# Performance work log

Measured on AMD Instinct MI355X. Metric: run time of the kernel, lower is better.

Reference implementation:

```python
import jax, jax.numpy as jnp
import numpy as np

DIM = 256
NUM_HEADS = 4
HEAD_DIM = DIM // NUM_HEADS
EPS = 1e-5


def setup_inputs() -> dict:
    key = jax.random.key(0)
    ks = jax.random.split(key, 8)
    B, N, C = 8, 2048, DIM
    s = 0.02
    return {
        "x": jax.random.normal(ks[0], (B, N, C), jnp.float32),
        "qkv_w": jax.random.normal(ks[1], (C, 3 * C), jnp.float32) * s,
        "qkv_b": jnp.zeros((3 * C,), jnp.float32),
        "proj_w": jax.random.normal(ks[2], (C, C), jnp.float32) * s,
        "proj_b": jnp.zeros((C,), jnp.float32),
        "ln1_g": jnp.ones((C,), jnp.float32),
        "ln1_b": jnp.zeros((C,), jnp.float32),
        "ln2_g": jnp.ones((C,), jnp.float32),
        "ln2_b": jnp.zeros((C,), jnp.float32),
        "mlp_w1": jax.random.normal(ks[3], (C, 2 * C), jnp.float32) * s,
        "mlp_b1": jnp.zeros((2 * C,), jnp.float32),
        "mlp_w2": jax.random.normal(ks[4], (2 * C, C), jnp.float32) * s,
        "mlp_b2": jnp.zeros((C,), jnp.float32),
    }


def _layernorm(x, g, b):
    mu = jnp.mean(x, axis=-1, keepdims=True)
    var = jnp.mean(jnp.square(x - mu), axis=-1, keepdims=True)
    return (x - mu) * jax.lax.rsqrt(var + EPS) * g + b


def reference(x, qkv_w, qkv_b, proj_w, proj_b, ln1_g, ln1_b, ln2_g, ln2_b,
              mlp_w1, mlp_b1, mlp_w2, mlp_b2):
    B, N, C = x.shape
    H, D = NUM_HEADS, HEAD_DIM
    shortcut = x
    h = _layernorm(x, ln1_g, ln1_b)
    qkv = (h @ qkv_w + qkv_b).reshape(B, N, 3, H, D)
    q = qkv[:, :, 0].transpose(0, 2, 1, 3)  # [B,H,N,D]
    k = qkv[:, :, 1].transpose(0, 2, 1, 3)
    v = qkv[:, :, 2].transpose(0, 2, 1, 3)
    attn = jnp.einsum('bhnd,bhmd->bhnm', q, k) * (D ** -0.5)
    attn = jax.nn.softmax(attn, axis=-1)  # dropout = identity (eval mode)
    o = jnp.einsum('bhnm,bhmd->bhnd', attn, v)
    o = o.transpose(0, 2, 1, 3).reshape(B, N, C)
    x = o @ proj_w + proj_b + shortcut
    h2 = _layernorm(x, ln2_g, ln2_b)
    mlp = jax.nn.gelu(h2 @ mlp_w1 + mlp_b1, approximate=False) @ mlp_w2 + mlp_b2
    return x + mlp
```

## Files before the change

### kernel.cpp

```cpp
#include <hip/hip_runtime.h>

typedef __bf16 bf16;
typedef __bf16 bf16x8 __attribute__((ext_vector_type(8)));
typedef __bf16 bf16x4 __attribute__((ext_vector_type(4)));
typedef float  f32x4  __attribute__((ext_vector_type(4)));
typedef unsigned u32x2 __attribute__((ext_vector_type(2)));

typedef __attribute__((address_space(1))) const void GASV;
typedef __attribute__((address_space(3))) void LASV;

__device__ __forceinline__ void gload16(const void* g, void* l) {
  __builtin_amdgcn_global_load_lds((GASV*)g, (LASV*)l, 16, 0, 0);
}

__global__ __launch_bounds__(256) void wconv_all(const float* __restrict__ qkv_w,
                                                 const float* __restrict__ proj_w,
                                                 const float* __restrict__ w1,
                                                 const float* __restrict__ w2,
                                                 bf16* __restrict__ Wtqkv,
                                                 bf16* __restrict__ WtP,
                                                 bf16* __restrict__ Wt1,
                                                 bf16* __restrict__ Wt2) {
  const int idx = blockIdx.x * 256 + threadIdx.x;
  if (idx < 196608) {
    const int k = idx & 255, n = idx >> 8;
    Wtqkv[idx] = (bf16)qkv_w[k * 768 + n];
  } else if (idx < 262144) {
    const int i = idx - 196608, k = i & 255, n = i >> 8;
    WtP[i] = (bf16)proj_w[k * 256 + n];
  } else if (idx < 393216) {
    const int i = idx - 262144, k = i & 255, n = i >> 8;
    Wt1[i] = (bf16)w1[k * 512 + n];
  } else {
    const int i = idx - 393216, k = i & 511, n = i >> 9;
    Wt2[i] = (bf16)w2[k * 256 + n];
  }
}

__global__ __launch_bounds__(256) void ln_fwd(const float* __restrict__ x,
                                              const float* __restrict__ gam,
                                              const float* __restrict__ bet,
                                              bf16* __restrict__ out) {
  const int lane = threadIdx.x & 63;
  const int w = threadIdx.x >> 6;
  const size_t row = (size_t)blockIdx.x * 4 + w;
  const float4 v = *(const float4*)(x + row * 256 + lane * 4);
  float s1 = v.x + v.y + v.z + v.w;
  float s2 = v.x * v.x + v.y * v.y + v.z * v.z + v.w * v.w;
#pragma unroll
  for (int m = 1; m < 64; m <<= 1) {
    s1 += __shfl_xor(s1, m);
    s2 += __shfl_xor(s2, m);
  }
  const float mu = s1 * (1.0f / 256.0f);
  const float var = s2 * (1.0f / 256.0f) - mu * mu;
  const float rs = rsqrtf(var + 1e-5f);
  const float4 g4 = *(const float4*)(gam + lane * 4);
  const float4 b4 = *(const float4*)(bet + lane * 4);
  bf16x4 o;
  o[0] = (bf16)((v.x - mu) * rs * g4.x + b4.x);
  o[1] = (bf16)((v.y - mu) * rs * g4.y + b4.y);
  o[2] = (bf16)((v.z - mu) * rs * g4.z + b4.z);
  o[3] = (bf16)((v.w - mu) * rs * g4.w + b4.w);
  *(bf16x4*)(out + row * 256 + lane * 4) = o;
}

template <int EPI>
__global__ __launch_bounds__(256) void gemm_bt(const bf16* __restrict__ A,
                                               const bf16* __restrict__ Bt,
                                               const float* __restrict__ bias,
                                               const float* __restrict__ res,
                                               void* __restrict__ outp,
                                               int M, int N, int K) {
  __shared__ bf16 Al[2][8192];
  __shared__ bf16 Bl[2][8192];
  const int tid = threadIdx.x;
  const int lane = tid & 63;
  const int wid = tid >> 6;
  const int wm = wid >> 1, wn = wid & 1;
  const int nbm = M >> 7;
  const int bm = (int)blockIdx.x % nbm;
  const int bn = (int)blockIdx.x / nbm;
  const int m0 = bm << 7, n0 = bn << 7;
  const int nk = K >> 6;

  f32x4 acc[4][4];
#pragma unroll
  for (int i = 0; i < 4; ++i)
#pragma unroll
    for (int j = 0; j < 4; ++j) acc[i][j] = (f32x4){0.f, 0.f, 0.f, 0.f};

  auto stage = [&](int t, int s) {
    const int k0 = t << 6;
#pragma unroll
    for (int p = 0; p < 4; ++p) {
      const int idx = p * 4096 + tid * 16;
      const int row = idx >> 7;
      const int colb = idx & 127;
      gload16((const char*)(A + ((size_t)(m0 + row) * K + k0)) + colb,
              (char*)&Al[s][0] + p * 4096 + ((tid >> 6) << 10));
      gload16((const char*)(Bt + ((size_t)(n0 + row) * K + k0)) + colb,
              (char*)&Bl[s][0] + p * 4096 + ((tid >> 6) << 10));
    }
  };

  stage(0, 0);
  asm volatile("s_waitcnt vmcnt(0)" ::: "memory");
  __syncthreads();

  for (int t = 0; t < nk; ++t) {
    if (t + 1 < nk) stage(t + 1, (t + 1) & 1);
    const bf16* pa = &Al[t & 1][0] + (wm * 64 + (lane & 15)) * 64 + ((lane >> 4) << 3);
    const bf16* pb = &Bl[t & 1][0] + (wn * 64 + (lane & 15)) * 64 + ((lane >> 4) << 3);
    bf16x8 av[4][2], bv[4][2];
#pragma unroll
    for (int f = 0; f < 4; ++f)
#pragma unroll
      for (int ks = 0; ks < 2; ++ks) {
        av[f][ks] = *(const bf16x8*)(pa + f * 1024 + ks * 32);
        bv[f][ks] = *(const bf16x8*)(pb + f * 1024 + ks * 32);
      }
    __builtin_amdgcn_s_setprio(1);
#pragma unroll
    for (int fm = 0; fm < 4; ++fm)
#pragma unroll
      for (int fn = 0; fn < 4; ++fn) {
        acc[fm][fn] = __builtin_amdgcn_mfma_f32_16x16x32_bf16(av[fm][0], bv[fn][0], acc[fm][fn], 0, 0, 0);
        acc[fm][fn] = __builtin_amdgcn_mfma_f32_16x16x32_bf16(av[fm][1], bv[fn][1], acc[fm][fn], 0, 0, 0);
      }
    __builtin_amdgcn_s_setprio(0);
    asm volatile("s_waitcnt vmcnt(0)" ::: "memory");
    __syncthreads();
  }

#pragma unroll
  for (int fm = 0; fm < 4; ++fm)
#pragma unroll
    for (int fn = 0; fn < 4; ++fn) {
      const int r0 = m0 + wm * 64 + fm * 16 + ((lane >> 4) << 2);
      const int c = n0 + wn * 64 + fn * 16 + (lane & 15);
#pragma unroll
      for (int j = 0; j < 4; ++j) {
        const int r = r0 + j;
        const float v = acc[fm][fn][j];
        if constexpr (EPI == 0) {
          ((bf16*)outp)[(size_t)r * N + c] = (bf16)(v + bias[c]);
        } else if constexpr (EPI == 1) {
          ((bf16*)outp)[(size_t)r * 2048 + ((size_t)(c >> 11)) * 524288 + (c & 2047)] =
              (bf16)(v + bias[r]);
        } else if constexpr (EPI == 2) {
          ((float*)outp)[(size_t)r * N + c] = v + bias[c] + res[(size_t)r * N + c];
        } else {
          const float u = v + bias[c];
          ((bf16*)outp)[(size_t)r * N + c] = (bf16)(u * 0.5f * (1.0f + erff(u * 0.70710678118f)));
        }
      }
    }
}

__global__ __launch_bounds__(256) void attn_fwd(const bf16* __restrict__ qk,
                                                const bf16* __restrict__ vT,
                                                bf16* __restrict__ ob) {
  __shared__ bf16 Kl[3][4096];
  __shared__ bf16 Vl[3][4096];
  __shared__ bf16 Pl[4][2048];
  const int tid = threadIdx.x;
  const int lane = tid & 63;
  const int w = tid >> 6;
  const int g = lane >> 4;
  const int qi = lane & 15;
  const int bh = blockIdx.x & 31;
  const int qt = blockIdx.x >> 5;
  const int b = bh >> 2, h = bh & 3;

  const size_t qrow0 = (size_t)b * 2048 + qt * 128 + w * 32 + qi;
  bf16x8 qf[2][2];
#pragma unroll
  for (int f = 0; f < 2; ++f) {
    const bf16* qp = qk + (qrow0 + f * 16) * 512 + h * 64 + g * 8;
    qf[f][0] = *(const bf16x8*)qp;
    qf[f][1] = *(const bf16x8*)(qp + 32);
  }

  float mrun[2] = {0.f, 0.f};
  float lsum[2] = {0.f, 0.f};
  f32x4 o[4][2];
#pragma unroll
  for (int i = 0; i < 4; ++i)
#pragma unroll
    for (int f = 0; f < 2; ++f) o[i][f] = (f32x4){0.f, 0.f, 0.f, 0.f};

  constexpr float CEXP = 0.125f * 1.44269504088896340736f;
  constexpr float THR = 8.0f / CEXP;

  const char* kbase = (const char*)qk + ((size_t)b * 2048) * 1024 + 512 + h * 128;
  const char* vbase = (const char*)vT + (size_t)bh * 262144;
  const char* ks[2];
  const char* vs[2];
#pragma unroll
  for (int i = 0; i < 2; ++i) {
    const int fk = i * 2 + (w >> 1);
    const int half = w & 1;
    ks[i] = kbase + (fk * 16 + qi) * 1024 + half * 64 + g * 16;
    vs[i] = vbase + (size_t)(fk * 16 + qi) * 4096 + half * 64 + g * 16;
  }
  char* const pw = (char*)&Pl[w][0];
  int paddr[4];
#pragma unroll
  for (int fk = 0; fk < 4; ++fk)
    paddr[fk] = (fk >> 1) * 2048 + ((fk & 1) * 2 + (g >> 1)) * 256 + qi * 16 + (g & 1) * 8;
  const char* const prd = (const char*)&Pl[w][0] + lane * 16;

  auto stage = [&](int slot) {
    char* kd = (char*)&Kl[0][0] + slot * 8192 + w * 1024;
    char* vd = (char*)&Vl[0][0] + slot * 8192 + w * 1024;
    gload16(ks[0], kd);
    gload16(ks[1], kd + 4096);
    gload16(vs[0], vd);
    gload16(vs[1], vd + 4096);
    ks[0] += 65536; ks[1] += 65536;
    vs[0] += 128;   vs[1] += 128;
  };

  stage(0);
  stage(1);
  asm volatile("s_waitcnt vmcnt(4)" ::: "memory");
  __builtin_amdgcn_s_barrier();

  int slot = 0, slot2 = 2;
  for (int t = 0; t < 32; ++t) {
    if (t < 30) stage(slot2);
    const char* kb = (const char*)&Kl[0][0] + slot * 8192 + lane * 16;
    f32x4 st[4][2];
    __builtin_amdgcn_s_setprio(1);
#pragma unroll
    for (int fk = 0; fk < 4; ++fk) {
      const bf16x8 k0 = *(const bf16x8*)(kb + fk * 2048);
      const bf16x8 k1 = *(const bf16x8*)(kb + fk * 2048 + 1024);
#pragma unroll
      for (int f = 0; f < 2; ++f) {
        f32x4 z = (f32x4){0.f, 0.f, 0.f, 0.f};
        st[fk][f] = __builtin_amdgcn_mfma_f32_16x16x32_bf16(k0, qf[f][0], z, 0, 0, 0);
        st[fk][f] = __builtin_amdgcn_mfma_f32_16x16x32_bf16(k1, qf[f][1], st[fk][f], 0, 0, 0);
      }
    }
    __builtin_amdgcn_s_setprio(0);
    float pmax[2];
#pragma unroll
    for (int f = 0; f < 2; ++f) {
      float m0 = fmaxf(fmaxf(st[0][f][0], st[0][f][1]), fmaxf(st[0][f][2], st[0][f][3]));
      float m1 = fmaxf(fmaxf(st[1][f][0], st[1][f][1]), fmaxf(st[1][f][2], st[1][f][3]));
      float m2 = fmaxf(fmaxf(st[2][f][0], st[2][f][1]), fmaxf(st[2][f][2], st[2][f][3]));
      float m3 = fmaxf(fmaxf(st[3][f][0], st[3][f][1]), fmaxf(st[3][f][2], st[3][f][3]));
      pmax[f] = fmaxf(fmaxf(m0, m1), fmaxf(m2, m3));
    }
    if (!__all(pmax[0] <= mrun[0] + THR && pmax[1] <= mrun[1] + THR)) {
#pragma unroll
      for (int f = 0; f < 2; ++f) {
        float mt = fmaxf(pmax[f], __shfl_xor(pmax[f], 16));
        mt = fmaxf(mt, __shfl_xor(mt, 32));
        const float mnew = fmaxf(mrun[f], mt);
        const float alpha = exp2f(CEXP * (mrun[f] - mnew));
        lsum[f] *= alpha;
#pragma unroll
        for (int fd = 0; fd < 4; ++fd)
#pragma unroll
          for (int j = 0; j < 4; ++j) o[fd][f][j] *= alpha;
        mrun[f] = mnew;
      }
    }
    unsigned pk[4][2][2];
#pragma unroll
    for (int f = 0; f < 2; ++f) {
      const float negcm = -CEXP * mrun[f];
      float ts = 0.f;
#pragma unroll
      for (int fk = 0; fk < 4; ++fk)
#pragma unroll
        for (int jp = 0; jp < 2; ++jp) {
          const float p0 = exp2f(fmaf(st[fk][f][2 * jp], CEXP, negcm));
          const float p1 = exp2f(fmaf(st[fk][f][2 * jp + 1], CEXP, negcm));
          ts += p0 + p1;
          union { bf16 h2[2]; unsigned u; } cv;
          cv.h2[0] = (bf16)p0;
          cv.h2[1] = (bf16)p1;
          pk[fk][f][jp] = cv.u;
        }
      lsum[f] += ts;
    }
#pragma unroll
    for (int fk = 0; fk < 4; ++fk) {
      u32x2 w0, w1;
      w0[0] = pk[fk][0][0]; w0[1] = pk[fk][0][1];
      w1[0] = pk[fk][1][0]; w1[1] = pk[fk][1][1];
      *(u32x2*)(pw + paddr[fk]) = w0;
      *(u32x2*)(pw + paddr[fk] + 1024) = w1;
    }
    bf16x8 pa[2][2];
#pragma unroll
    for (int f = 0; f < 2; ++f)
#pragma unroll
      for (int ksl = 0; ksl < 2; ++ksl)
        pa[f][ksl] = *(const bf16x8*)(prd + ksl * 2048 + f * 1024);
    const char* vb = (const char*)&Vl[0][0] + slot * 8192 + lane * 16;
    __builtin_amdgcn_s_setprio(1);
#pragma unroll
    for (int fd = 0; fd < 4; ++fd) {
      const bf16x8 v0 = *(const bf16x8*)(vb + fd * 2048);
      const bf16x8 v1 = *(const bf16x8*)(vb + fd * 2048 + 1024);
#pragma unroll
      for (int f = 0; f < 2; ++f) {
        o[fd][f] = __builtin_amdgcn_mfma_f32_16x16x32_bf16(v0, pa[f][0], o[fd][f], 0, 0, 0);
        o[fd][f] = __builtin_amdgcn_mfma_f32_16x16x32_bf16(v1, pa[f][1], o[fd][f], 0, 0, 0);
      }
    }
    __builtin_amdgcn_s_setprio(0);
    if (t < 30) {
      asm volatile("s_waitcnt vmcnt(4)" ::: "memory");
    } else {
      asm volatile("s_waitcnt vmcnt(0)" ::: "memory");
    }
    __builtin_amdgcn_s_barrier();
    slot = (slot == 2) ? 0 : slot + 1;
    slot2 = (slot2 == 2) ? 0 : slot2 + 1;
  }

#pragma unroll
  for (int f = 0; f < 2; ++f) {
    float l = lsum[f];
    l += __shfl_xor(l, 16);
    l += __shfl_xor(l, 32);
    lsum[f] = 1.0f / l;
  }
#pragma unroll
  for (int f = 0; f < 2; ++f) {
    bf16* const orow = ob + (qrow0 + f * 16) * 256 + h * 64 + g * 4;
#pragma unroll
    for (int fd = 0; fd < 4; ++fd) {
      bf16x4 ov;
#pragma unroll
      for (int j = 0; j < 4; ++j) ov[j] = (bf16)(o[fd][f][j] * lsum[f]);
      *(bf16x4*)(orow + fd * 16) = ov;
    }
  }
}

extern "C" void kernel_launch(void* const* d_in, const int* in_sizes, int n_in,
                              void* d_out, int out_size, void* d_ws, size_t ws_size,
                              hipStream_t stream) {
  const float* x      = (const float*)d_in[0];
  const float* qkv_w  = (const float*)d_in[1];
  const float* qkv_b  = (const float*)d_in[2];
  const float* proj_w = (const float*)d_in[3];
  const float* proj_b = (const float*)d_in[4];
  const float* ln1_g  = (const float*)d_in[5];
  const float* ln1_b  = (const float*)d_in[6];
  const float* ln2_g  = (const float*)d_in[7];
  const float* ln2_b  = (const float*)d_in[8];
  const float* mlp_w1 = (const float*)d_in[9];
  const float* mlp_b1 = (const float*)d_in[10];
  const float* mlp_w2 = (const float*)d_in[11];
  const float* mlp_b2 = (const float*)d_in[12];
  float* out = (float*)d_out;

  char* ws = (char*)d_ws;
  bf16* Wtqkv = (bf16*)(ws);
  bf16* WtP   = (bf16*)(ws + 393216);
  bf16* Wt1   = (bf16*)(ws + 524288);
  bf16* Wt2   = (bf16*)(ws + 786432);
  bf16* h     = (bf16*)(ws + 1048576);
  bf16* qkb   = (bf16*)(ws + 9437184);
  bf16* vT    = (bf16*)(ws + 26214400);
  bf16* obuf  = (bf16*)(ws + 34603008);
  float* x2   = (float*)(ws + 42991616);
  bf16* a1 = qkb;
  bf16* h2 = h;

  wconv_all<<<2048, 256, 0, stream>>>(qkv_w, proj_w, mlp_w1, mlp_w2, Wtqkv, WtP, Wt1, Wt2);

  ln_fwd<<<4096, 256, 0, stream>>>(x, ln1_g, ln1_b, h);
  gemm_bt<0><<<512, 256, 0, stream>>>(h, Wtqkv, qkv_b, nullptr, qkb, 16384, 512, 256);
  gemm_bt<1><<<256, 256, 0, stream>>>(Wtqkv + 512 * 256, h, qkv_b + 512, nullptr, vT, 256, 16384, 256);
  attn_fwd<<<512, 256, 0, stream>>>(qkb, vT, obuf);
  gemm_bt<2><<<256, 256, 0, stream>>>(obuf, WtP, proj_b, x, x2, 16384, 256, 256);
  ln_fwd<<<4096, 256, 0, stream>>>(x2, ln2_g, ln2_b, h2);
  gemm_bt<3><<<512, 256, 0, stream>>>(h2, Wt1, mlp_b1, nullptr, a1, 16384, 512, 256);
  gemm_bt<2><<<256, 256, 0, stream>>>(a1, Wt2, mlp_b2, x2, out, 16384, 256, 512);
}
```

Baseline: 171.4 us.

## Split attention KV range across two wave groups and merge softmax partials

Attention blocks now launch 512 threads as two groups of four waves. Each group processes alternating 64-key tiles of the same 128 query rows, with its own double-buffered K/V slabs. At the end, the groups exchange running max, sum and half of the output accumulators through shared memory and combine them with a flash-decoding style rescale. The P-to-V stage is also split into two k-slices so the P scratch buffer shrinks. The aim is more waves in flight per block to hide latency, at the cost of an extra merge phase, a full vmcnt(0) wait each iteration and reduced prefetch depth.

Result: slower. 198.0 us (+15.5%).

```diff
diff --git a/kernel.cpp b/kernel.cpp
--- a/kernel.cpp
+++ b/kernel.cpp
@@ -158,22 +158,24 @@
     }
 }
 
-__global__ __launch_bounds__(256) void attn_fwd(const bf16* __restrict__ qk,
-                                                const bf16* __restrict__ vT,
-                                                bf16* __restrict__ ob) {
-  __shared__ bf16 Kl[3][4096];
-  __shared__ bf16 Vl[3][4096];
-  __shared__ bf16 Pl[4][2048];
+__global__ __launch_bounds__(512, 4) void attn_fwd(const bf16* __restrict__ qk,
+                                                   const bf16* __restrict__ vT,
+                                                   bf16* __restrict__ ob) {
+  __shared__ bf16 Kl[2][2][4096];
+  __shared__ bf16 Vl[2][2][4096];
+  __shared__ bf16 Pl[8][1024];
   const int tid = threadIdx.x;
   const int lane = tid & 63;
   const int w = tid >> 6;
+  const int grp = w >> 2;
+  const int wq = w & 3;
   const int g = lane >> 4;
   const int qi = lane & 15;
   const int bh = blockIdx.x & 31;
   const int qt = blockIdx.x >> 5;
   const int b = bh >> 2, h = bh & 3;
 
-  const size_t qrow0 = (size_t)b * 2048 + qt * 128 + w * 32 + qi;
+  const size_t qrow0 = (size_t)b * 2048 + qt * 128 + wq * 32 + qi;
   bf16x8 qf[2][2];
 #pragma unroll
   for (int f = 0; f < 2; ++f) {
@@ -199,38 +201,38 @@
   const char* vs[2];
 #pragma unroll
   for (int i = 0; i < 2; ++i) {
-    const int fk = i * 2 + (w >> 1);
-    const int half = w & 1;
-    ks[i] = kbase + (fk * 16 + qi) * 1024 + half * 64 + g * 16;
-    vs[i] = vbase + (size_t)(fk * 16 + qi) * 4096 + half * 64 + g * 16;
-  }
+    const int fk = i * 2 + (wq >> 1);
+    const int half = wq & 1;
+    ks[i] = kbase + (size_t)grp * 65536 + (fk * 16 + qi) * 1024 + half * 64 + g * 16;
+    vs[i] = vbase + (size_t)grp * 128 + (size_t)(fk * 16 + qi) * 4096 + half * 64 + g * 16;
+  }
+  char* const kslab = (char*)&Kl[grp][0][0];
+  char* const vslab = (char*)&Vl[grp][0][0];
   char* const pw = (char*)&Pl[w][0];
-  int paddr[4];
-#pragma unroll
-  for (int fk = 0; fk < 4; ++fk)
-    paddr[fk] = (fk >> 1) * 2048 + ((fk & 1) * 2 + (g >> 1)) * 256 + qi * 16 + (g & 1) * 8;
-  const char* const prd = (const char*)&Pl[w][0] + lane * 16;
+  int paddrb[2];
+#pragma unroll
+  for (int bb = 0; bb < 2; ++bb)
+    paddrb[bb] = (bb * 2 + (g >> 1)) * 256 + qi * 16 + (g & 1) * 8;
+  const char* const prd = pw + lane * 16;
 
   auto stage = [&](int slot) {
-    char* kd = (char*)&Kl[0][0] + slot * 8192 + w * 1024;
-    char* vd = (char*)&Vl[0][0] + slot * 8192 + w * 1024;
+    char* kd = kslab + slot * 8192 + wq * 1024;
+    char* vd = vslab + slot * 8192 + wq * 1024;
     gload16(ks[0], kd);
     gload16(ks[1], kd + 4096);
     gload16(vs[0], vd);
     gload16(vs[1], vd + 4096);
-    ks[0] += 65536; ks[1] += 65536;
-    vs[0] += 128;   vs[1] += 128;
+    ks[0] += 131072; ks[1] += 131072;
+    vs[0] += 256;    vs[1] += 256;
   };
 
   stage(0);
-  stage(1);
-  asm volatile("s_waitcnt vmcnt(4)" ::: "memory");
+  asm volatile("s_waitcnt vmcnt(0)" ::: "memory");
   __builtin_amdgcn_s_barrier();
 
-  int slot = 0, slot2 = 2;
-  for (int t = 0; t < 32; ++t) {
-    if (t < 30) stage(slot2);
-    const char* kb = (const char*)&Kl[0][0] + slot * 8192 + lane * 16;
+  for (int t = 0; t < 16; ++t) {
+    if (t < 15) stage((t + 1) & 1);
+    const char* kb = kslab + (t & 1) * 8192 + lane * 16;
     f32x4 st[4][2];
     __builtin_amdgcn_s_setprio(1);
 #pragma unroll
@@ -288,41 +290,35 @@
         }
       lsum[f] += ts;
     }
-#pragma unroll
-    for (int fk = 0; fk < 4; ++fk) {
-      u32x2 w0, w1;
-      w0[0] = pk[fk][0][0]; w0[1] = pk[fk][0][1];
-      w1[0] = pk[fk][1][0]; w1[1] = pk[fk][1][1];
-      *(u32x2*)(pw + paddr[fk]) = w0;
-      *(u32x2*)(pw + paddr[fk] + 1024) = w1;
-    }
-    bf16x8 pa[2][2];
-#pragma unroll
-    for (int f = 0; f < 2; ++f)
-#pragma unroll
-      for (int ksl = 0; ksl < 2; ++ksl)
-        pa[f][ksl] = *(const bf16x8*)(prd + ksl * 2048 + f * 1024);
-    const char* vb = (const char*)&Vl[0][0] + slot * 8192 + lane * 16;
-    __builtin_amdgcn_s_setprio(1);
-#pragma unroll
-    for (int fd = 0; fd < 4; ++fd) {
-      const bf16x8 v0 = *(const bf16x8*)(vb + fd * 2048);
-      const bf16x8 v1 = *(const bf16x8*)(vb + fd * 2048 + 1024);
-#pragma unroll
-      for (int f = 0; f < 2; ++f) {
-        o[fd][f] = __builtin_amdgcn_mfma_f32_16x16x32_bf16(v0, pa[f][0], o[fd][f], 0, 0, 0);
-        o[fd][f] = __builtin_amdgcn_mfma_f32_16x16x32_bf16(v1, pa[f][1], o[fd][f], 0, 0, 0);
-      }
-    }
-    __builtin_amdgcn_s_setprio(0);
-    if (t < 30) {
-      asm volatile("s_waitcnt vmcnt(4)" ::: "memory");
-    } else {
-      asm volatile("s_waitcnt vmcnt(0)" ::: "memory");
-    }
+    const char* vb = vslab + (t & 1) * 8192 + lane * 16;
+#pragma unroll
+    for (int ksl = 0; ksl < 2; ++ksl) {
+#pragma unroll
+      for (int bb = 0; bb < 2; ++bb) {
+        const int fk = 2 * ksl + bb;
+#pragma unroll
+        for (int f = 0; f < 2; ++f) {
+          u32x2 pv2;
+          pv2[0] = pk[fk][f][0];
+          pv2[1] = pk[fk][f][1];
+          *(u32x2*)(pw + f * 1024 + paddrb[bb]) = pv2;
+        }
+      }
+      bf16x8 pa[2];
+#pragma unroll
+      for (int f = 0; f < 2; ++f) pa[f] = *(const bf16x8*)(prd + f * 1024);
+      __builtin_amdgcn_s_setprio(1);
+#pragma unroll
+      for (int fd = 0; fd < 4; ++fd) {
+        const bf16x8 vv = *(const bf16x8*)(vb + fd * 2048 + ksl * 1024);
+#pragma unroll
+        for (int f = 0; f < 2; ++f)
+          o[fd][f] = __builtin_amdgcn_mfma_f32_16x16x32_bf16(vv, pa[f], o[fd][f], 0, 0, 0);
+      }
+      __builtin_amdgcn_s_setprio(0);
+    }
+    asm volatile("s_waitcnt vmcnt(0)" ::: "memory");
     __builtin_amdgcn_s_barrier();
-    slot = (slot == 2) ? 0 : slot + 1;
-    slot2 = (slot2 == 2) ? 0 : slot2 + 1;
   }
 
 #pragma unroll
@@ -330,17 +326,40 @@
     float l = lsum[f];
     l += __shfl_xor(l, 16);
     l += __shfl_xor(l, 32);
-    lsum[f] = 1.0f / l;
-  }
+    lsum[f] = l;
+  }
+  f32x4 stv;
+  stv[0] = mrun[0]; stv[1] = lsum[0]; stv[2] = mrun[1]; stv[3] = lsum[1];
+  *(f32x4*)((char*)&Pl[0][0] + w * 1024 + lane * 16) = stv;
+  char* const oslab = (char*)&Kl[0][0][0] + w * 4096;
+#pragma unroll
+  for (int fd2 = 0; fd2 < 2; ++fd2) {
+    const int wf = grp ? fd2 : 2 + fd2;
+#pragma unroll
+    for (int f = 0; f < 2; ++f)
+      *(f32x4*)(oslab + (fd2 * 2 + f) * 1024 + lane * 16) = o[wf][f];
+  }
+  __syncthreads();
+  const int p = w ^ 4;
+  const f32x4 pst = *(const f32x4*)((char*)&Pl[0][0] + p * 1024 + lane * 16);
+  const char* const pslab = (char*)&Kl[0][0][0] + p * 4096;
 #pragma unroll
   for (int f = 0; f < 2; ++f) {
-    bf16* const orow = ob + (qrow0 + f * 16) * 256 + h * 64 + g * 4;
-#pragma unroll
-    for (int fd = 0; fd < 4; ++fd) {
+    const float mme = mrun[f], lme = lsum[f];
+    const float mot = pst[2 * f], lot = pst[2 * f + 1];
+    const float ms = fmaxf(mme, mot);
+    const float am = exp2f(CEXP * (mme - ms));
+    const float ao = exp2f(CEXP * (mot - ms));
+    const float inv = 1.0f / (lme * am + lot * ao);
+#pragma unroll
+    for (int fd2 = 0; fd2 < 2; ++fd2) {
+      const int kf = grp ? 2 + fd2 : fd2;
+      const f32x4 po = *(const f32x4*)(pslab + (fd2 * 2 + f) * 1024 + lane * 16);
       bf16x4 ov;
 #pragma unroll
-      for (int j = 0; j < 4; ++j) ov[j] = (bf16)(o[fd][f][j] * lsum[f]);
-      *(bf16x4*)(orow + fd * 16) = ov;
+      for (int j = 0; j < 4; ++j)
+        ov[j] = (bf16)((o[kf][f][j] * am + po[j] * ao) * inv);
+      *(bf16x4*)(ob + (qrow0 + f * 16) * 256 + h * 64 + kf * 16 + g * 4) = ov;
     }
   }
 }
@@ -381,7 +400,7 @@
   ln_fwd<<<4096, 256, 0, stream>>>(x, ln1_g, ln1_b, h);
   gemm_bt<0><<<512, 256, 0, stream>>>(h, Wtqkv, qkv_b, nullptr, qkb, 16384, 512, 256);
   gemm_bt<1><<<256, 256, 0, stream>>>(Wtqkv + 512 * 256, h, qkv_b + 512, nullptr, vT, 256, 16384, 256);
-  attn_fwd<<<512, 256, 0, stream>>>(qkb, vT, obuf);
+  attn_fwd<<<512, 512, 0, stream>>>(qkb, vT, obuf);
   gemm_bt<2><<<256, 256, 0, stream>>>(obuf, WtP, proj_b, x, x2, 16384, 256, 256);
   ln_fwd<<<4096, 256, 0, stream>>>(x2, ln2_g, ln2_b, h2);
   gemm_bt<3><<<512, 256, 0, stream>>>(h2, Wt1, mlp_b1, nullptr, a1, 16384, 512, 256);
```
